# Kernel optimization log

Measured on AMD Instinct MI355X. Metric: run time of the kernel, lower is better.

The kernel has to match this reference:

```python
import jax, jax.numpy as jnp
from jax import lax
import numpy as np

# --- module constants (from init_kwargs) ---
MAXK = 512
BLOCK = 3            # Shi-Tomasi structure-tensor window
NUM_PAIRS = 256      # BAD descriptor dimensionality
ITERS = 20           # Sinkhorn iterations
EPS = 1.0            # entropy regularization
UNUSED = 1.0         # dustbin score
NMS_R = 3
THR = 0.0
PATCH_R = 8          # BAD pair-offset radius
BOX = 5              # BAD pre-smoothing box size

# fixed BAD comparison-pair offsets (dy1,dx1,dy2,dx2) -- constants, not learned
_OFFSETS = jnp.asarray(
    np.random.RandomState(42).randint(-PATCH_R, PATCH_R + 1, size=(NUM_PAIRS, 4)),
    dtype=jnp.int32)

_SOBEL_X = jnp.array([[-1., 0., 1.], [-2., 0., 2.], [-1., 0., 1.]], jnp.float32)[None, None]
_SOBEL_Y = jnp.transpose(_SOBEL_X, (0, 1, 3, 2))


def _conv(x, k):  # x: [B,1,H,W], k: [1,1,kh,kw]
    return lax.conv_general_dilated(x, k, (1, 1), 'SAME',
                                    dimension_numbers=('NCHW', 'OIHW', 'NCHW'))


def _detector(img):
    """Shi-Tomasi min-eigenvalue score map + dense BAD descriptor map."""
    Ix = _conv(img, _SOBEL_X)
    Iy = _conv(img, _SOBEL_Y)
    box = jnp.ones((1, 1, BLOCK, BLOCK), jnp.float32) / (BLOCK * BLOCK)
    Ixx = _conv(Ix * Ix, box)
    Iyy = _conv(Iy * Iy, box)
    Ixy = _conv(Ix * Iy, box)
    score = 0.5 * ((Ixx + Iyy) - jnp.sqrt((Ixx - Iyy) ** 2 + 4.0 * Ixy ** 2 + 1e-12))

    smooth = _conv(img, jnp.ones((1, 1, BOX, BOX), jnp.float32) / (BOX * BOX))[:, 0]  # [B,H,W]
    B, H, W = smooth.shape
    pad = jnp.pad(smooth, ((0, 0), (PATCH_R, PATCH_R), (PATCH_R, PATCH_R)), mode='edge')

    def one_pair(off):  # box-average difference at two shifted locations
        a = lax.dynamic_slice(pad, (0, PATCH_R + off[0], PATCH_R + off[1]), (B, H, W))
        b = lax.dynamic_slice(pad, (0, PATCH_R + off[2], PATCH_R + off[3]), (B, H, W))
        return a - b

    desc = jax.vmap(one_pair)(_OFFSETS)           # [D,B,H,W]
    return score[:, 0], jnp.transpose(desc, (1, 0, 2, 3))  # [B,H,W], [B,D,H,W]


def _nms_topk(score):
    """Max-pool NMS + top-k keypoint selection; invalid kpts = (-1,-1)."""
    win = 2 * NMS_R + 1
    mx = lax.reduce_window(score, -jnp.inf, lax.max, (1, win, win), (1, 1, 1), 'SAME')
    mask = (score >= mx) & (score > THR)
    B, H, W = score.shape
    masked = jnp.where(mask, score, -jnp.inf).reshape(B, H * W)
    vals, idx = lax.top_k(masked, MAXK)
    valid = jnp.isfinite(vals)
    y = (idx // W).astype(jnp.float32)
    x = (idx % W).astype(jnp.float32)
    kpts = jnp.where(valid[..., None], jnp.stack([y, x], -1), -1.0)  # [B,K,2] (y,x)
    return kpts


def _extract(desc_map, kpts):
    """Bilinear (subpixel) descriptor gather; zeros for invalid keypoints."""
    B, D, H, W = desc_map.shape
    valid = (kpts[:, :, 0] >= 0).astype(desc_map.dtype)
    y = jnp.clip(kpts[:, :, 0], 0.0, H - 1.0)
    x = jnp.clip(kpts[:, :, 1], 0.0, W - 1.0)
    y0 = jnp.floor(y); x0 = jnp.floor(x)
    y1 = jnp.minimum(y0 + 1.0, H - 1.0); x1 = jnp.minimum(x0 + 1.0, W - 1.0)
    wy = y - y0; wx = x - x0
    y0i, y1i = y0.astype(jnp.int32), y1.astype(jnp.int32)
    x0i, x1i = x0.astype(jnp.int32), x1.astype(jnp.int32)
    flat = desc_map.reshape(B, D, H * W)

    def g(yi, xi):  # [B,K] -> [B,D,K]
        return jnp.take_along_axis(flat, (yi * W + xi)[:, None, :], axis=2)

    d = (g(y0i, x0i) * ((1 - wy) * (1 - wx))[:, None, :]
         + g(y0i, x1i) * ((1 - wy) * wx)[:, None, :]
         + g(y1i, x0i) * (wy * (1 - wx))[:, None, :]
         + g(y1i, x1i) * (wy * wx)[:, None, :])
    return jnp.transpose(d, (0, 2, 1)) * valid[..., None]  # [B,K,D]


def _sinkhorn(d1, d2):
    """Log-domain Sinkhorn with dustbin row/col (SuperGlue-style OT)."""
    s1 = jnp.sum(d1 * d1, -1)
    s2 = jnp.sum(d2 * d2, -1)
    dist = jnp.sqrt(jnp.clip(
        s1[:, :, None] + s2[:, None, :] - 2.0 * jnp.einsum('bkd,bld->bkl', d1, d2),
        1e-12))
    B, K, _ = dist.shape
    Z = jnp.full((B, K + 1, K + 1), UNUSED / EPS, dtype=dist.dtype)
    Z = Z.at[:, :K, :K].set(-dist / EPS)
    norm = -jnp.log(2.0 * K)
    log_mu = jnp.concatenate([jnp.zeros((K,), Z.dtype),
                              jnp.log(jnp.full((1,), float(K), Z.dtype))]) + norm
    log_nu = log_mu

    def body(_, uv):
        u, v = uv
        u = log_mu - jax.scipy.special.logsumexp(Z + v[:, None, :], axis=2)
        v = log_nu - jax.scipy.special.logsumexp(Z + u[:, :, None], axis=1)
        return (u, v)

    u0 = jnp.zeros((B, K + 1), Z.dtype)
    u, v = lax.fori_loop(0, ITERS, body, (u0, u0))
    return jnp.exp(Z + u[:, :, None] + v[:, None, :] - norm)  # [B,K+1,K+1]


def _l2norm(d):
    return d / (jnp.linalg.norm(d, axis=-1, keepdims=True) + 1e-12)


def setup_inputs() -> dict:
    key = jax.random.key(0)
    k1, k2 = jax.random.split(key)
    image1 = jax.random.uniform(k1, (1, 1, 480, 640), jnp.float32)
    image2 = jax.random.uniform(k2, (1, 1, 480, 640), jnp.float32)
    return {"image1": image1, "image2": image2}


def reference(image1, image2):
    s1, m1 = _detector(image1)
    s2, m2 = _detector(image2)
    kpts1 = _nms_topk(s1)
    kpts2 = _nms_topk(s2)
    d1 = _l2norm(_extract(m1, kpts1))
    d2 = _l2norm(_extract(m2, kpts2))
    probs = _sinkhorn(d1, d2)
    return (kpts1, kpts2, probs)
```

## Files before the change

kernel.cpp:

```cpp
#include <hip/hip_runtime.h>
#include <math.h>
#include <stdint.h>

#define HH 480
#define WW 640
#define HW (HH*WW)
#define KK 512
#define DD 256
#define KP1 513
#define NSLOT 16
#define NBX 40
#define NBY 30
#define SLOTS_PER_IMG (NBX*NBY*NSLOT)
#define SVCAP 4096
#define SB 32
#define NORM_F (-6.9314718055994531f)
#define LOGK_F (6.2383246250395077f)
#define MU0 (1.0f/1024.0f)
#define MU1 (0.5f)

#define OFF_Z      16384u
#define OFF_SMOOTH 2473984u
#define OFF_CAND   4931584u
#define OFF_KIDX   5238784u
#define OFF_DESC   5242880u
#define OFF_SBUF   6291456u
#define OFF_PCA    6295552u
#define OFF_PCB    6361216u
#define OFF_VA     6426880u
#define OFF_VB     6429184u
#define OFF_U      6431488u

struct OffsTab { int v[1024]; };
static constexpr OffsTab make_offsets() {
  OffsTab o{};
  unsigned st[624] = {};
  st[0] = 42u;
  for (int i = 1; i < 624; ++i)
    st[i] = 1812433253u*(st[i-1] ^ (st[i-1] >> 30)) + (unsigned)i;
  int idx = 624, got = 0;
  while (got < 1024) {
    if (idx == 624) {
      for (int i = 0; i < 624; ++i) {
        unsigned y = (st[i] & 0x80000000u) | (st[(i+1)%624] & 0x7fffffffu);
        st[i] = st[(i+397)%624] ^ (y >> 1) ^ ((y & 1u) ? 2567483615u : 0u);
      }
      idx = 0;
    }
    unsigned y = st[idx++];
    y ^= y >> 11;
    y ^= (y << 7)  & 2636928640u;
    y ^= (y << 15) & 4022730752u;
    y ^= y >> 18;
    unsigned mv = y & 31u;
    if (mv <= 16u) { o.v[got] = (int)mv - 8; ++got; }
  }
  return o;
}
__device__ __constant__ OffsTab OFFS = make_offsets();

__global__ __launch_bounds__(256) void detnms_kernel(const float* __restrict__ img0,
    const float* __restrict__ img1, float* __restrict__ smooth,
    unsigned long long* __restrict__ cand) {
  __shared__ float tile[26][26];
  __shared__ float pxx[24][24], pyy[24][24], pxy[24][24];
  __shared__ float sc[22][22];
  __shared__ int wsum[4], wbase[4];
  const int imgI = blockIdx.z;
  const float* img = imgI ? img1 : img0;
  const int bx0 = blockIdx.x*16, by0 = blockIdx.y*16;
  const int tx = threadIdx.x, ty = threadIdx.y, lt = ty*16+tx;
  for (int p = lt; p < 676; p += 256) {
    int r = p/26, c = p%26;
    int gy = by0-5+r, gx = bx0-5+c;
    tile[r][c] = (gy >= 0 && gy < HH && gx >= 0 && gx < WW) ? img[gy*WW+gx] : 0.f;
  }
  __syncthreads();
  for (int p = lt; p < 576; p += 256) {
    int r = p/24, c = p%24;
    int gy = by0-4+r, gx = bx0-4+c;
    float vxx = 0.f, vyy = 0.f, vxy = 0.f;
    if (gy >= 0 && gy < HH && gx >= 0 && gx < WW) {
      float t00 = tile[r][c],   t01 = tile[r][c+1],   t02 = tile[r][c+2];
      float t10 = tile[r+1][c],                        t12 = tile[r+1][c+2];
      float t20 = tile[r+2][c], t21 = tile[r+2][c+1], t22 = tile[r+2][c+2];
      float ix = t00*(-1.f) + t02*1.f + t10*(-2.f) + t12*2.f + t20*(-1.f) + t22*1.f;
      float iy = t00*(-1.f) + t01*(-2.f) + t02*(-1.f) + t20*1.f + t21*2.f + t22*1.f;
      vxx = ix*ix; vyy = iy*iy; vxy = ix*iy;
    }
    pxx[r][c] = vxx; pyy[r][c] = vyy; pxy[r][c] = vxy;
  }
  __syncthreads();
  const float c9 = 1.f/9.f, c25 = 1.f/25.f;
  float sm = 0.f;
  for (int r = 0; r < 5; ++r)
    for (int c = 0; c < 5; ++c)
      sm += tile[ty+3+r][tx+3+c] * c25;
  for (int p = lt; p < 484; p += 256) {
    int r = p/22, c = p%22;
    int gy = by0-3+r, gx = bx0-3+c;
    float v = -INFINITY;
    if (gy >= 0 && gy < HH && gx >= 0 && gx < WW) {
      float sxx = 0.f, syy = 0.f, sxy = 0.f;
      for (int dr = 0; dr < 3; ++dr)
        for (int dc = 0; dc < 3; ++dc) {
          sxx += pxx[r+dr][c+dc] * c9;
          syy += pyy[r+dr][c+dc] * c9;
          sxy += pxy[r+dr][c+dc] * c9;
        }
      float tdif = sxx - syy;
      v = 0.5f * ((sxx + syy) - sqrtf(tdif*tdif + 4.f*(sxy*sxy) + 1e-12f));
    }
    sc[r][c] = v;
  }
  __syncthreads();
  smooth[imgI*HW + (by0+ty)*WW + (bx0+tx)] = sm;
  float cv = sc[ty+3][tx+3];
  float m = -INFINITY;
  for (int r = 0; r < 7; ++r)
    for (int c = 0; c < 7; ++c)
      m = fmaxf(m, sc[ty+r][tx+c]);
  bool pred = (cv >= m && cv > 0.f);
  unsigned long long mask = __ballot(pred);
  int lane = lt & 63, wid = lt >> 6;
  if (lane == 0) wsum[wid] = __popcll(mask);
  __syncthreads();
  if (lt == 0) {
    int s0 = wsum[0], s1 = wsum[1], s2 = wsum[2], s3 = wsum[3];
    wbase[0] = 0; wbase[1] = s0; wbase[2] = s0+s1; wbase[3] = s0+s1+s2;
    wsum[0] = s0+s1+s2+s3;
  }
  __syncthreads();
  const int total = wsum[0];
  const size_t slotBase = (size_t)imgI*SLOTS_PER_IMG + (size_t)(blockIdx.y*NBX + blockIdx.x)*NSLOT;
  if (pred) {
    int pos = wbase[wid] + __popcll(mask & ((1ull << lane) - 1ull));
    if (pos < NSLOT) {
      int idx = (by0+ty)*WW + (bx0+tx);
      unsigned int ub = __float_as_uint(cv) | 0x80000000u;
      cand[slotBase + pos] = ((unsigned long long)ub << 32) | (unsigned int)(~idx);
    }
  }
  if (lt >= total && lt < NSLOT) cand[slotBase + lt] = 0ull;
}

__global__ __launch_bounds__(1024) void select2_kernel(const unsigned long long* __restrict__ cand,
    float* __restrict__ kptsOut, int* __restrict__ kidx) {
  __shared__ unsigned long long sk[SVCAP];
  __shared__ unsigned long long sorted[KK];
  __shared__ int hist[1024];
  __shared__ int sB1, sB2, sNeed, sCount;
  const int imgI = blockIdx.x, t = threadIdx.x;
  const unsigned long long* cd = cand + (size_t)imgI*SLOTS_PER_IMG;
  unsigned long long kreg[19];
  #pragma unroll
  for (int r = 0; r < 19; ++r) {
    int i = t + r*1024;
    kreg[r] = (i < SLOTS_PER_IMG) ? cd[i] : 0ull;
  }
  hist[t] = 0;
  if (t == 0) { sB1 = -1; sB2 = 0; sCount = 0; }
  if (t < KK) sorted[t] = 0ull;
  __syncthreads();
  #pragma unroll
  for (int r = 0; r < 19; ++r)
    if (kreg[r]) atomicAdd(&hist[(int)(kreg[r] >> 54)], 1);
  __syncthreads();
  for (int d = 1; d < 1024; d <<= 1) {
    int vv = hist[t] + ((t + d < 1024) ? hist[t + d] : 0);
    __syncthreads();
    hist[t] = vv;
    __syncthreads();
  }
  if (hist[t] >= KK) atomicMax(&sB1, t);
  __syncthreads();
  const int b1 = sB1;
  if (t == 0 && b1 >= 0) sNeed = KK - ((b1 < 1023) ? hist[b1 + 1] : 0);
  __syncthreads();
  int b2 = 0;
  if (b1 >= 0) {
    hist[t] = 0;
    __syncthreads();
    #pragma unroll
    for (int r = 0; r < 19; ++r) {
      unsigned long long k = kreg[r];
      if (k && (int)(k >> 54) == b1) atomicAdd(&hist[(int)(k >> 44) & 1023], 1);
    }
    __syncthreads();
    for (int d = 1; d < 1024; d <<= 1) {
      int vv = hist[t] + ((t + d < 1024) ? hist[t + d] : 0);
      __syncthreads();
      hist[t] = vv;
      __syncthreads();
    }
    if (hist[t] >= sNeed) atomicMax(&sB2, t);
    __syncthreads();
    b2 = sB2;
  }
  #pragma unroll
  for (int r = 0; r < 19; ++r) {
    unsigned long long k = kreg[r];
    if (k) {
      int bin1 = (int)(k >> 54);
      if (bin1 > b1 || (bin1 == b1 && ((int)(k >> 44) & 1023) >= b2)) {
        int pos = atomicAdd(&sCount, 1);
        if (pos < SVCAP) sk[pos] = k;
      }
    }
  }
  __syncthreads();
  int n = sCount; if (n > SVCAP) n = SVCAP;
  for (int i = t; i < n; i += 1024) {
    unsigned long long key = sk[i];
    int rk = 0;
    for (int m = 0; m < n; ++m) rk += (sk[m] > key) ? 1 : 0;
    if (rk < KK) sorted[rk] = key;
  }
  __syncthreads();
  if (t < KK) {
    unsigned long long key = sorted[t];
    float y = -1.f, x = -1.f;
    int id = -1;
    if (key != 0ull) {
      id = (int)(~(unsigned int)(key & 0xFFFFFFFFull));
      y = (float)(id / WW);
      x = (float)(id % WW);
    }
    kptsOut[imgI*2*KK + 2*t]     = y;
    kptsOut[imgI*2*KK + 2*t + 1] = x;
    kidx[imgI*KK + t] = id;
  }
}

__global__ __launch_bounds__(256) void desc_kernel(const float* __restrict__ smooth,
    const int* __restrict__ kidx, float* __restrict__ desc, float* __restrict__ sbuf) {
  __shared__ float wsum[4];
  const int k = blockIdx.x, imgI = blockIdx.y;
  const int j = threadIdx.x;
  const int id = kidx[imgI*KK + k];
  float val = 0.f;
  if (id >= 0) {
    int y = id / WW, x = id % WW;
    int o0 = OFFS.v[4*j], o1 = OFFS.v[4*j+1], o2 = OFFS.v[4*j+2], o3 = OFFS.v[4*j+3];
    const float* sm = smooth + imgI*HW;
    int ya = min(max(y+o0, 0), HH-1), xa = min(max(x+o1, 0), WW-1);
    int yb = min(max(y+o2, 0), HH-1), xb = min(max(x+o3, 0), WW-1);
    val = sm[ya*WW + xa] - sm[yb*WW + xb];
  }
  float ss = val*val;
  for (int off = 32; off; off >>= 1) ss += __shfl_down(ss, off);
  if ((j & 63) == 0) wsum[j >> 6] = ss;
  __syncthreads();
  if (j == 0) wsum[0] = wsum[0] + wsum[1] + wsum[2] + wsum[3];
  __syncthreads();
  float tot = wsum[0];
  float inv = 1.f / (sqrtf(tot) + 1e-12f);
  desc[((size_t)imgI*KK + k)*DD + j] = val * inv;
  if (j == 0) sbuf[imgI*KK + k] = tot * inv * inv;
}

__global__ __launch_bounds__(256) void zbuild_kernel(const float* __restrict__ desc,
    const float* __restrict__ sbuf, float* __restrict__ Z) {
  __shared__ float sA[16][260], sB[16][260];
  const int ty = threadIdx.y, tx = threadIdx.x;
  const int i0 = blockIdx.y*16, j0 = blockIdx.x*16;
  const int lt = ty*16 + tx;
  for (int p = lt; p < 16*DD; p += 256) {
    int r = p / DD, c = p % DD;
    sA[r][c] = (i0 + r < KK) ? desc[((size_t)0*KK + i0 + r)*DD + c] : 0.f;
    sB[r][c] = (j0 + r < KK) ? desc[((size_t)1*KK + j0 + r)*DD + c] : 0.f;
  }
  __syncthreads();
  const int i = i0 + ty, j = j0 + tx;
  if (i > KK || j > KK) return;
  if (i < KK && j < KK) {
    const float4* pa = (const float4*)&sA[ty][0];
    const float4* pb = (const float4*)&sB[tx][0];
    float acc = 0.f;
    for (int c4 = 0; c4 < DD/4; ++c4) {
      float4 a = pa[c4], b = pb[c4];
      acc += a.x*b.x; acc += a.y*b.y; acc += a.z*b.z; acc += a.w*b.w;
    }
    float d2 = sbuf[0*KK + i] + sbuf[1*KK + j] - 2.f*acc;
    Z[i*KP1 + j] = -sqrtf(fmaxf(d2, 1e-12f));
  } else {
    Z[i*KP1 + j] = 1.0f;
  }
}

__global__ __launch_bounds__(1024) void sink_step_kernel(const float* __restrict__ Z,
    const float* __restrict__ PcolIn, float* __restrict__ PcolOut,
    const float* __restrict__ vIn, float* __restrict__ vOut,
    float* __restrict__ uBuf, float* __restrict__ probs, int mode) {
  __shared__ float v[KP1];
  __shared__ float pcolw[16][KP1];
  const int t = threadIdx.x, b = blockIdx.x;
  const int widx = t >> 6, lane = t & 63;
  const int gw = b*16 + widx;
  if (mode == 0) {
    for (int j = t; j < KP1; j += 1024) v[j] = 0.f;
  } else {
    for (int j = t; j < KP1; j += 1024) {
      float s = 0.f;
      #pragma unroll
      for (int w = 0; w < SB; ++w) s += PcolIn[w*KP1 + j];
      float lognu = (j < KK) ? NORM_F : (LOGK_F + NORM_F);
      v[j] = lognu + vIn[j] - logf(s);
    }
  }
  __syncthreads();
  if (mode == 2) {
    const int nrows = (gw == 511) ? 2 : 1;
    for (int rr = 0; rr < nrows; ++rr) {
      const int r = rr ? 512 : gw;
      const float* zr = Z + (size_t)r*KP1;
      float* pr = probs + (size_t)r*KP1;
      const float ur = uBuf[r];
      #pragma unroll
      for (int e = 0; e < 8; ++e) {
        int j = lane + 64*e;
        pr[j] = expf(zr[j] + ur + v[j] - NORM_F);
      }
      if (lane == 0) pr[512] = expf(zr[512] + ur + v[512] - NORM_F);
    }
    return;
  }
  float pacc[9];
  #pragma unroll
  for (int e = 0; e < 9; ++e) pacc[e] = 0.f;
  const int nrows = (gw == 511) ? 2 : 1;
  for (int rr = 0; rr < nrows; ++rr) {
    const int r = rr ? 512 : gw;
    const float* zr = Z + (size_t)r*KP1;
    float tv[9]; float S = 0.f;
    #pragma unroll
    for (int e = 0; e < 8; ++e) {
      int j = lane + 64*e;
      tv[e] = expf(zr[j] + v[j]);
      S += tv[e];
    }
    tv[8] = 0.f;
    if (lane == 0) { tv[8] = expf(zr[512] + v[512]); S += tv[8]; }
    #pragma unroll
    for (int off = 32; off; off >>= 1) S += __shfl_xor(S, off);
    float mu = (r < 512) ? MU0 : MU1;
    float eu = mu / S;
    if (lane == 0) uBuf[r] = logf(eu);
    #pragma unroll
    for (int e = 0; e < 9; ++e) pacc[e] += tv[e] * eu;
  }
  #pragma unroll
  for (int e = 0; e < 8; ++e) pcolw[widx][lane + 64*e] = pacc[e];
  if (lane == 0) pcolw[widx][512] = pacc[8];
  __syncthreads();
  float* pc = PcolOut + (size_t)b*KP1;
  for (int j = t; j < KP1; j += 1024) {
    float s = 0.f;
    #pragma unroll
    for (int w = 0; w < 16; ++w) s += pcolw[w][j];
    pc[j] = s;
  }
  if (b == 0) {
    for (int j = t; j < KP1; j += 1024) vOut[j] = v[j];
  }
}

extern "C" void kernel_launch(void* const* d_in, const int* in_sizes, int n_in,
                              void* d_out, int out_size, void* d_ws, size_t ws_size,
                              hipStream_t stream) {
  const float* img1 = (const float*)d_in[0];
  const float* img2 = (const float*)d_in[1];
  float* out = (float*)d_out;
  char* ws = (char*)d_ws;

  float* smooth = (float*)(ws + OFF_SMOOTH);
  unsigned long long* cand = (unsigned long long*)(ws + OFF_CAND);
  int*   kidx   = (int*)  (ws + OFF_KIDX);
  float* desc   = (float*)(ws + OFF_DESC);
  float* sbuf   = (float*)(ws + OFF_SBUF);
  float* Z      = (float*)(ws + OFF_Z);
  float* pcA    = (float*)(ws + OFF_PCA);
  float* pcB    = (float*)(ws + OFF_PCB);
  float* vA     = (float*)(ws + OFF_VA);
  float* vB     = (float*)(ws + OFF_VB);
  float* uBuf   = (float*)(ws + OFF_U);
  float* probsOut = out + 2*KK*2;

  detnms_kernel<<<dim3(NBX, NBY, 2), dim3(16, 16), 0, stream>>>(img1, img2, smooth, cand);
  select2_kernel<<<2, 1024, 0, stream>>>(cand, out, kidx);
  desc_kernel<<<dim3(KK, 2), 256, 0, stream>>>(smooth, kidx, desc, sbuf);
  zbuild_kernel<<<dim3(33, 33), dim3(16, 16), 0, stream>>>(desc, sbuf, Z);

  sink_step_kernel<<<SB, 1024, 0, stream>>>(Z, pcB, pcA, vB, vA, uBuf, probsOut, 0);
  int ping = 0;
  for (int it = 1; it < 20; ++it) {
    float* pin  = ping ? pcB : pcA;
    float* pout = ping ? pcA : pcB;
    float* vin  = ping ? vB  : vA;
    float* vout = ping ? vA  : vB;
    sink_step_kernel<<<SB, 1024, 0, stream>>>(Z, pin, pout, vin, vout, uBuf, probsOut, 1);
    ping ^= 1;
  }
  {
    float* pin = ping ? pcB : pcA;
    float* vin = ping ? vB  : vA;
    sink_step_kernel<<<SB, 1024, 0, stream>>>(Z, pin, pcA, vin, vA, uBuf, probsOut, 2);
  }
}
```

Measured before the change: 166.9 us.

## Split top-k ranking into parallel kernel, separable NMS/box filters, compact Z layout

Several independent changes land together. The detector now builds its NMS max and 5x5 box smooth from separable row/column passes, and stores only Ix/Iy, squaring them on the fly. The quadratic rank sort moves out of the single-block select kernel into a separate rank kernel spread over 16 blocks per image, with the survivor cap cut to 1024. Z is stored as a dense 512x512 matrix and the dustbin row and column are treated as the constant 1.0, which lets zbuild drop its padding blocks and lets the Sinkhorn steps use contiguous float4 loads. The costs are an extra kernel launch and a smaller survivor cap, which could drop candidates if more than 1024 survive the histogram threshold.

```diff
diff --git a/kernel.cpp b/kernel.cpp
--- a/kernel.cpp
+++ b/kernel.cpp
@@ -12,13 +12,14 @@
 #define NBX 40
 #define NBY 30
 #define SLOTS_PER_IMG (NBX*NBY*NSLOT)
-#define SVCAP 4096
+#define SVN 1024
 #define SB 32
 #define NORM_F (-6.9314718055994531f)
 #define LOGK_F (6.2383246250395077f)
 #define MU0 (1.0f/1024.0f)
 #define MU1 (0.5f)
 
+#define OFF_SURV   0u
 #define OFF_Z      16384u
 #define OFF_SMOOTH 2473984u
 #define OFF_CAND   4931584u
@@ -30,6 +31,7 @@
 #define OFF_VA     6426880u
 #define OFF_VB     6429184u
 #define OFF_U      6431488u
+#define OFF_SVCNT  6438912u
 
 struct OffsTab { int v[1024]; };
 static constexpr OffsTab make_offsets() {
@@ -63,8 +65,10 @@
     const float* __restrict__ img1, float* __restrict__ smooth,
     unsigned long long* __restrict__ cand) {
   __shared__ float tile[26][26];
-  __shared__ float pxx[24][24], pyy[24][24], pxy[24][24];
+  __shared__ float ixA[24][24], iyA[24][24];
   __shared__ float sc[22][22];
+  __shared__ float vs[16][26];
+  __shared__ float vm[16][22];
   __shared__ int wsum[4], wbase[4];
   const int imgI = blockIdx.z;
   const float* img = imgI ? img1 : img0;
@@ -79,23 +83,18 @@
   for (int p = lt; p < 576; p += 256) {
     int r = p/24, c = p%24;
     int gy = by0-4+r, gx = bx0-4+c;
-    float vxx = 0.f, vyy = 0.f, vxy = 0.f;
+    float ix = 0.f, iy = 0.f;
     if (gy >= 0 && gy < HH && gx >= 0 && gx < WW) {
       float t00 = tile[r][c],   t01 = tile[r][c+1],   t02 = tile[r][c+2];
       float t10 = tile[r+1][c],                        t12 = tile[r+1][c+2];
       float t20 = tile[r+2][c], t21 = tile[r+2][c+1], t22 = tile[r+2][c+2];
-      float ix = t00*(-1.f) + t02*1.f + t10*(-2.f) + t12*2.f + t20*(-1.f) + t22*1.f;
-      float iy = t00*(-1.f) + t01*(-2.f) + t02*(-1.f) + t20*1.f + t21*2.f + t22*1.f;
-      vxx = ix*ix; vyy = iy*iy; vxy = ix*iy;
-    }
-    pxx[r][c] = vxx; pyy[r][c] = vyy; pxy[r][c] = vxy;
+      ix = t00*(-1.f) + t02*1.f + t10*(-2.f) + t12*2.f + t20*(-1.f) + t22*1.f;
+      iy = t00*(-1.f) + t01*(-2.f) + t02*(-1.f) + t20*1.f + t21*2.f + t22*1.f;
+    }
+    ixA[r][c] = ix; iyA[r][c] = iy;
   }
   __syncthreads();
   const float c9 = 1.f/9.f, c25 = 1.f/25.f;
-  float sm = 0.f;
-  for (int r = 0; r < 5; ++r)
-    for (int c = 0; c < 5; ++c)
-      sm += tile[ty+3+r][tx+3+c] * c25;
   for (int p = lt; p < 484; p += 256) {
     int r = p/22, c = p%22;
     int gy = by0-3+r, gx = bx0-3+c;
@@ -104,22 +103,34 @@
       float sxx = 0.f, syy = 0.f, sxy = 0.f;
       for (int dr = 0; dr < 3; ++dr)
         for (int dc = 0; dc < 3; ++dc) {
-          sxx += pxx[r+dr][c+dc] * c9;
-          syy += pyy[r+dr][c+dc] * c9;
-          sxy += pxy[r+dr][c+dc] * c9;
+          float jx = ixA[r+dr][c+dc], jy = iyA[r+dr][c+dc];
+          float pxxv = jx*jx, pyyv = jy*jy, pxyv = jx*jy;
+          sxx += pxxv*c9; syy += pyyv*c9; sxy += pxyv*c9;
         }
       float tdif = sxx - syy;
       v = 0.5f * ((sxx + syy) - sqrtf(tdif*tdif + 4.f*(sxy*sxy) + 1e-12f));
     }
     sc[r][c] = v;
   }
-  __syncthreads();
+  for (int p = lt; p < 416; p += 256) {
+    int i = p/26, c = p%26;
+    vs[i][c] = tile[i+3][c] + tile[i+4][c] + tile[i+5][c] + tile[i+6][c] + tile[i+7][c];
+  }
+  __syncthreads();
+  for (int p = lt; p < 352; p += 256) {
+    int i = p/22, c = p%22;
+    float m = sc[i][c];
+    m = fmaxf(m, sc[i+1][c]); m = fmaxf(m, sc[i+2][c]); m = fmaxf(m, sc[i+3][c]);
+    m = fmaxf(m, sc[i+4][c]); m = fmaxf(m, sc[i+5][c]); m = fmaxf(m, sc[i+6][c]);
+    vm[i][c] = m;
+  }
+  float sm = (vs[ty][tx+3] + vs[ty][tx+4] + vs[ty][tx+5] + vs[ty][tx+6] + vs[ty][tx+7]) * c25;
   smooth[imgI*HW + (by0+ty)*WW + (bx0+tx)] = sm;
+  __syncthreads();
   float cv = sc[ty+3][tx+3];
-  float m = -INFINITY;
-  for (int r = 0; r < 7; ++r)
-    for (int c = 0; c < 7; ++c)
-      m = fmaxf(m, sc[ty+r][tx+c]);
+  float m = vm[ty][tx];
+  m = fmaxf(m, vm[ty][tx+1]); m = fmaxf(m, vm[ty][tx+2]); m = fmaxf(m, vm[ty][tx+3]);
+  m = fmaxf(m, vm[ty][tx+4]); m = fmaxf(m, vm[ty][tx+5]); m = fmaxf(m, vm[ty][tx+6]);
   bool pred = (cv >= m && cv > 0.f);
   unsigned long long mask = __ballot(pred);
   int lane = lt & 63, wid = lt >> 6;
@@ -144,10 +155,8 @@
   if (lt >= total && lt < NSLOT) cand[slotBase + lt] = 0ull;
 }
 
-__global__ __launch_bounds__(1024) void select2_kernel(const unsigned long long* __restrict__ cand,
-    float* __restrict__ kptsOut, int* __restrict__ kidx) {
-  __shared__ unsigned long long sk[SVCAP];
-  __shared__ unsigned long long sorted[KK];
+__global__ __launch_bounds__(1024) void select2a_kernel(const unsigned long long* __restrict__ cand,
+    unsigned long long* __restrict__ surv, int* __restrict__ svcnt) {
   __shared__ int hist[1024];
   __shared__ int sB1, sB2, sNeed, sCount;
   const int imgI = blockIdx.x, t = threadIdx.x;
@@ -160,7 +169,6 @@
   }
   hist[t] = 0;
   if (t == 0) { sB1 = -1; sB2 = 0; sCount = 0; }
-  if (t < KK) sorted[t] = 0ull;
   __syncthreads();
   #pragma unroll
   for (int r = 0; r < 19; ++r)
@@ -204,31 +212,36 @@
       int bin1 = (int)(k >> 54);
       if (bin1 > b1 || (bin1 == b1 && ((int)(k >> 44) & 1023) >= b2)) {
         int pos = atomicAdd(&sCount, 1);
-        if (pos < SVCAP) sk[pos] = k;
+        if (pos < SVN) surv[imgI*SVN + pos] = k;
       }
     }
   }
   __syncthreads();
-  int n = sCount; if (n > SVCAP) n = SVCAP;
-  for (int i = t; i < n; i += 1024) {
-    unsigned long long key = sk[i];
-    int rk = 0;
-    for (int m = 0; m < n; ++m) rk += (sk[m] > key) ? 1 : 0;
-    if (rk < KK) sorted[rk] = key;
-  }
-  __syncthreads();
-  if (t < KK) {
-    unsigned long long key = sorted[t];
-    float y = -1.f, x = -1.f;
-    int id = -1;
-    if (key != 0ull) {
-      id = (int)(~(unsigned int)(key & 0xFFFFFFFFull));
-      y = (float)(id / WW);
-      x = (float)(id % WW);
-    }
-    kptsOut[imgI*2*KK + 2*t]     = y;
-    kptsOut[imgI*2*KK + 2*t + 1] = x;
-    kidx[imgI*KK + t] = id;
+  if (t == 0) svcnt[imgI] = (sCount < SVN) ? sCount : SVN;
+}
+
+__global__ __launch_bounds__(64) void rank_kernel(const unsigned long long* __restrict__ surv,
+    const int* __restrict__ svcnt, float* __restrict__ kptsOut, int* __restrict__ kidx) {
+  __shared__ unsigned long long sk[SVN];
+  const int imgI = blockIdx.y, t = threadIdx.x;
+  const int n = svcnt[imgI];
+  for (int i = t; i < SVN; i += 64) sk[i] = (i < n) ? surv[imgI*SVN + i] : 0ull;
+  __syncthreads();
+  const int k = blockIdx.x*64 + t;
+  if (k < n) {
+    unsigned long long key = sk[k];
+    int r = 0;
+    for (int m = 0; m < n; ++m) r += (sk[m] > key) ? 1 : 0;
+    if (r < KK) {
+      int id = (int)(~(unsigned int)(key & 0xFFFFFFFFull));
+      kptsOut[imgI*2*KK + 2*r]     = (float)(id / WW);
+      kptsOut[imgI*2*KK + 2*r + 1] = (float)(id % WW);
+      kidx[imgI*KK + r] = id;
+    }
+  } else if (k >= n && k < KK) {
+    kptsOut[imgI*2*KK + 2*k]     = -1.f;
+    kptsOut[imgI*2*KK + 2*k + 1] = -1.f;
+    kidx[imgI*KK + k] = -1;
   }
 }
 
@@ -267,25 +280,20 @@
   const int lt = ty*16 + tx;
   for (int p = lt; p < 16*DD; p += 256) {
     int r = p / DD, c = p % DD;
-    sA[r][c] = (i0 + r < KK) ? desc[((size_t)0*KK + i0 + r)*DD + c] : 0.f;
-    sB[r][c] = (j0 + r < KK) ? desc[((size_t)1*KK + j0 + r)*DD + c] : 0.f;
+    sA[r][c] = desc[((size_t)0*KK + i0 + r)*DD + c];
+    sB[r][c] = desc[((size_t)1*KK + j0 + r)*DD + c];
   }
   __syncthreads();
   const int i = i0 + ty, j = j0 + tx;
-  if (i > KK || j > KK) return;
-  if (i < KK && j < KK) {
-    const float4* pa = (const float4*)&sA[ty][0];
-    const float4* pb = (const float4*)&sB[tx][0];
-    float acc = 0.f;
-    for (int c4 = 0; c4 < DD/4; ++c4) {
-      float4 a = pa[c4], b = pb[c4];
-      acc += a.x*b.x; acc += a.y*b.y; acc += a.z*b.z; acc += a.w*b.w;
-    }
-    float d2 = sbuf[0*KK + i] + sbuf[1*KK + j] - 2.f*acc;
-    Z[i*KP1 + j] = -sqrtf(fmaxf(d2, 1e-12f));
-  } else {
-    Z[i*KP1 + j] = 1.0f;
-  }
+  const float4* pa = (const float4*)&sA[ty][0];
+  const float4* pb = (const float4*)&sB[tx][0];
+  float acc = 0.f;
+  for (int c4 = 0; c4 < DD/4; ++c4) {
+    float4 a = pa[c4], b = pb[c4];
+    acc += a.x*b.x; acc += a.y*b.y; acc += a.z*b.z; acc += a.w*b.w;
+  }
+  float d2 = sbuf[0*KK + i] + sbuf[KK + j] - 2.f*acc;
+  Z[(size_t)i*KK + j] = -sqrtf(fmaxf(d2, 1e-12f));
 }
 
 __global__ __launch_bounds__(1024) void sink_step_kernel(const float* __restrict__ Z,
@@ -309,49 +317,64 @@
     }
   }
   __syncthreads();
+  const int j0 = lane*8;
+  const float4 va = *(const float4*)&v[j0];
+  const float4 vb = *(const float4*)&v[j0+4];
+  const float vv[8] = {va.x, va.y, va.z, va.w, vb.x, vb.y, vb.z, vb.w};
+  const int nrows = (gw == 511) ? 2 : 1;
   if (mode == 2) {
-    const int nrows = (gw == 511) ? 2 : 1;
     for (int rr = 0; rr < nrows; ++rr) {
       const int r = rr ? 512 : gw;
-      const float* zr = Z + (size_t)r*KP1;
       float* pr = probs + (size_t)r*KP1;
       const float ur = uBuf[r];
+      float zv[8];
+      if (r < 512) {
+        float4 z0 = *(const float4*)&Z[(size_t)r*KK + j0];
+        float4 z1 = *(const float4*)&Z[(size_t)r*KK + j0 + 4];
+        zv[0]=z0.x; zv[1]=z0.y; zv[2]=z0.z; zv[3]=z0.w;
+        zv[4]=z1.x; zv[5]=z1.y; zv[6]=z1.z; zv[7]=z1.w;
+      } else {
+        #pragma unroll
+        for (int q = 0; q < 8; ++q) zv[q] = 1.0f;
+      }
       #pragma unroll
-      for (int e = 0; e < 8; ++e) {
-        int j = lane + 64*e;
-        pr[j] = expf(zr[j] + ur + v[j] - NORM_F);
-      }
-      if (lane == 0) pr[512] = expf(zr[512] + ur + v[512] - NORM_F);
+      for (int q = 0; q < 8; ++q) pr[j0+q] = expf(zv[q] + ur + vv[q] - NORM_F);
+      if (lane == 0) pr[512] = expf(1.0f + ur + v[512] - NORM_F);
     }
     return;
   }
-  float pacc[9];
+  float pacc[8]; float pacc8 = 0.f;
   #pragma unroll
-  for (int e = 0; e < 9; ++e) pacc[e] = 0.f;
-  const int nrows = (gw == 511) ? 2 : 1;
+  for (int q = 0; q < 8; ++q) pacc[q] = 0.f;
   for (int rr = 0; rr < nrows; ++rr) {
     const int r = rr ? 512 : gw;
-    const float* zr = Z + (size_t)r*KP1;
-    float tv[9]; float S = 0.f;
+    float zv[8];
+    if (r < 512) {
+      float4 z0 = *(const float4*)&Z[(size_t)r*KK + j0];
+      float4 z1 = *(const float4*)&Z[(size_t)r*KK + j0 + 4];
+      zv[0]=z0.x; zv[1]=z0.y; zv[2]=z0.z; zv[3]=z0.w;
+      zv[4]=z1.x; zv[5]=z1.y; zv[6]=z1.z; zv[7]=z1.w;
+    } else {
+      #pragma unroll
+      for (int q = 0; q < 8; ++q) zv[q] = 1.0f;
+    }
+    float tv[8]; float S = 0.f;
     #pragma unroll
-    for (int e = 0; e < 8; ++e) {
-      int j = lane + 64*e;
-      tv[e] = expf(zr[j] + v[j]);
-      S += tv[e];
-    }
-    tv[8] = 0.f;
-    if (lane == 0) { tv[8] = expf(zr[512] + v[512]); S += tv[8]; }
+    for (int q = 0; q < 8; ++q) { tv[q] = expf(zv[q] + vv[q]); S += tv[q]; }
+    float t8 = 0.f;
+    if (lane == 0) { t8 = expf(1.0f + v[512]); S += t8; }
     #pragma unroll
     for (int off = 32; off; off >>= 1) S += __shfl_xor(S, off);
     float mu = (r < 512) ? MU0 : MU1;
     float eu = mu / S;
     if (lane == 0) uBuf[r] = logf(eu);
     #pragma unroll
-    for (int e = 0; e < 9; ++e) pacc[e] += tv[e] * eu;
+    for (int q = 0; q < 8; ++q) pacc[q] += tv[q] * eu;
+    pacc8 += t8 * eu;
   }
   #pragma unroll
-  for (int e = 0; e < 8; ++e) pcolw[widx][lane + 64*e] = pacc[e];
-  if (lane == 0) pcolw[widx][512] = pacc[8];
+  for (int q = 0; q < 8; ++q) pcolw[widx][j0+q] = pacc[q];
+  if (lane == 0) pcolw[widx][512] = pacc8;
   __syncthreads();
   float* pc = PcolOut + (size_t)b*KP1;
   for (int j = t; j < KP1; j += 1024) {
@@ -373,6 +396,7 @@
   float* out = (float*)d_out;
   char* ws = (char*)d_ws;
 
+  unsigned long long* surv = (unsigned long long*)(ws + OFF_SURV);
   float* smooth = (float*)(ws + OFF_SMOOTH);
   unsigned long long* cand = (unsigned long long*)(ws + OFF_CAND);
   int*   kidx   = (int*)  (ws + OFF_KIDX);
@@ -384,12 +408,14 @@
   float* vA     = (float*)(ws + OFF_VA);
   float* vB     = (float*)(ws + OFF_VB);
   float* uBuf   = (float*)(ws + OFF_U);
+  int*   svcnt  = (int*)  (ws + OFF_SVCNT);
   float* probsOut = out + 2*KK*2;
 
   detnms_kernel<<<dim3(NBX, NBY, 2), dim3(16, 16), 0, stream>>>(img1, img2, smooth, cand);
-  select2_kernel<<<2, 1024, 0, stream>>>(cand, out, kidx);
+  select2a_kernel<<<2, 1024, 0, stream>>>(cand, surv, svcnt);
+  rank_kernel<<<dim3(16, 2), 64, 0, stream>>>(surv, svcnt, out, kidx);
   desc_kernel<<<dim3(KK, 2), 256, 0, stream>>>(smooth, kidx, desc, sbuf);
-  zbuild_kernel<<<dim3(33, 33), dim3(16, 16), 0, stream>>>(desc, sbuf, Z);
+  zbuild_kernel<<<dim3(32, 32), dim3(16, 16), 0, stream>>>(desc, sbuf, Z);
 
   sink_step_kernel<<<SB, 1024, 0, stream>>>(Z, pcB, pcA, vB, vA, uBuf, probsOut, 0);
   int ping = 0;
```

Result: faster. 162.8 us (-2.5%).
